# Performance work log

Measured on AMD Instinct MI355X. Metric: run time of the kernel, lower is better.

## Reference

```python
import math
import jax, jax.numpy as jnp
import numpy as np

EMB = 1024
HEADS = 16
HEAD_DIM = EMB // HEADS


def setup_inputs() -> dict:
    key = jax.random.key(0)
    ks = jax.random.split(key, 6)
    b, l = 4, 4096
    x = jax.random.normal(ks[0], (b, l, EMB), dtype=jnp.float32)
    # torch Linear weight shape (out, in); xavier_normal std = sqrt(2/(in+out))
    std = math.sqrt(2.0 / (EMB + EMB))
    Wq = jax.random.normal(ks[1], (EMB, EMB), dtype=jnp.float32) * std
    Wk = jax.random.normal(ks[2], (EMB, EMB), dtype=jnp.float32) * std
    Wv = jax.random.normal(ks[3], (EMB, EMB), dtype=jnp.float32) * std
    Wu = jax.random.normal(ks[4], (EMB, EMB), dtype=jnp.float32) * std
    Wo = jax.random.normal(ks[5], (EMB, EMB), dtype=jnp.float32) * std
    return {"x": x, "Wq": Wq, "Wk": Wk, "Wv": Wv, "Wu": Wu, "Wo": Wo}


def _srms_norm(x, eps=1e-12):
    # SRMSNorm over last dim with scale 1/sqrt(head_dims), computed in fp32
    dtype = x.dtype
    xf = x.astype(jnp.float32)
    scale = 1.0 / math.sqrt(x.shape[-1])
    n = jnp.linalg.norm(xf * scale, axis=-1, keepdims=True)
    return (xf / jnp.maximum(n, eps)).astype(dtype)


def reference(x, Wq, Wk, Wv, Wu, Wo):
    b, l, d = x.shape
    h, hd = HEADS, HEAD_DIM
    scale = math.sqrt(hd)

    def proj(W):
        return jnp.einsum('bld,ed->ble', x, W).reshape(b, l, h, hd).transpose(0, 2, 1, 3)

    q = jax.nn.relu(proj(Wq)) / scale        # (b,h,l,hd)
    k = jax.nn.relu(proj(Wk)) / scale
    v = proj(Wv)
    u = jax.nn.silu(proj(Wu))

    kv = jnp.einsum('bhlk,bhlv->bhkv', k, v)  # (b,h,hd,hd) state
    out = jnp.einsum('bhlk,bhkv->bhlv', q, kv)
    out = _srms_norm(out) * u
    out = out.transpose(0, 2, 1, 3).reshape(b, l, d)
    return jnp.einsum('bld,ed->ble', out, Wo)
```

## Files before the change

### kernel.cpp

```cpp
#include <hip/hip_runtime.h>

typedef _Float16 f16;
typedef _Float16 f16x4 __attribute__((ext_vector_type(4)));
typedef _Float16 f16x8 __attribute__((ext_vector_type(8)));
typedef float f32x4 __attribute__((ext_vector_type(4)));

#define EMB 1024
#define SEQL 4096
#define BATCH 4
#define NH 16
#define HD 64
#define BH 64
#define MROWS 16384
#define KVSPLIT 16

#define GLOAD_LDS(gp, lp) \
    __builtin_amdgcn_global_load_lds((const __attribute__((address_space(1))) void*)(gp), \
                                     (__attribute__((address_space(3))) void*)(lp), 16, 0, 0)

__global__ void cvt_kernel(const float* __restrict__ in, f16* __restrict__ out, int n4) {
    int i = blockIdx.x * blockDim.x + threadIdx.x;
    if (i < n4) {
        float4 v = ((const float4*)in)[i];
        f16x4 o = { (f16)v.x, (f16)v.y, (f16)v.z, (f16)v.w };
        ((f16x4*)out)[i] = o;
    }
}

struct WPtrs { const float* p[5]; };

__global__ void cvt_w_kernel(WPtrs wp, f16* __restrict__ out) {
    int i = blockIdx.x * blockDim.x + threadIdx.x;
    int wsel = blockIdx.y;
    const float4* src = (const float4*)wp.p[wsel];
    float4 v = src[i];
    f16x4 o = { (f16)v.x, (f16)v.y, (f16)v.z, (f16)v.w };
    ((f16x4*)(out + (size_t)wsel * EMB * EMB))[i] = o;
}

__global__ void zero_kernel(float4* __restrict__ p, int n4) {
    int i = blockIdx.x * blockDim.x + threadIdx.x;
    if (i < n4) p[i] = float4{0.f, 0.f, 0.f, 0.f};
}

template<int MODE>
__global__ __launch_bounds__(256) void gemm_kernel(
    const f16* __restrict__ A, const f16* __restrict__ Bt,
    void* __restrict__ Cv, int M, int N, int K)
{
    __shared__ f16 As[128 * 32];
    __shared__ f16 Bs[128 * 32];

    const int lane = threadIdx.x & 63;
    const int w    = threadIdx.x >> 6;
    const int rw   = lane & 15;
    const int quad = lane >> 4;
    const int m0 = blockIdx.y * 128;
    const int n0 = blockIdx.x * 128;
    const int mw = (w >> 1) * 64;
    const int nw = (w & 1) * 64;

    const int srow = lane >> 2;
    const int scol = (((lane & 3) ^ ((lane >> 3) & 3)) * 8);
    const f16* ag0 = A  + (size_t)(m0 + w * 16 + srow) * K + scol;
    const f16* ag1 = A  + (size_t)(m0 + 64 + w * 16 + srow) * K + scol;
    const f16* bg0 = Bt + (size_t)(n0 + w * 16 + srow) * K + scol;
    const f16* bg1 = Bt + (size_t)(n0 + 64 + w * 16 + srow) * K + scol;
    f16* la0 = &As[(w * 16) * 32];
    f16* la1 = &As[(64 + w * 16) * 32];
    f16* lb0 = &Bs[(w * 16) * 32];
    f16* lb1 = &Bs[(64 + w * 16) * 32];

    const int swz = (quad ^ ((rw >> 1) & 3)) * 8;

    f32x4 acc[4][4] = {};

    for (int k0 = 0; k0 < K; k0 += 32) {
        __syncthreads();
        GLOAD_LDS(ag0 + k0, la0);
        GLOAD_LDS(ag1 + k0, la1);
        GLOAD_LDS(bg0 + k0, lb0);
        GLOAD_LDS(bg1 + k0, lb1);
        __syncthreads();

        f16x8 af[4], bf[4];
        #pragma unroll
        for (int i = 0; i < 4; i++)
            af[i] = *(const f16x8*)&As[(mw + 16 * i + rw) * 32 + swz];
        #pragma unroll
        for (int j = 0; j < 4; j++)
            bf[j] = *(const f16x8*)&Bs[(nw + 16 * j + rw) * 32 + swz];
        #pragma unroll
        for (int i = 0; i < 4; i++)
            #pragma unroll
            for (int j = 0; j < 4; j++)
                acc[i][j] = __builtin_amdgcn_mfma_f32_16x16x32_f16(bf[j], af[i], acc[i][j], 0, 0, 0);
    }

    #pragma unroll
    for (int i = 0; i < 4; i++) {
        #pragma unroll
        for (int j = 0; j < 4; j++) {
            const int m_idx = m0 + mw + 16 * i + rw;
            const int n_idx = n0 + nw + 16 * j + quad * 4;
            if (MODE == 0) {
                float4 vv = { acc[i][j][0], acc[i][j][1], acc[i][j][2], acc[i][j][3] };
                *(float4*)&((float*)Cv)[(size_t)m_idx * N + n_idx] = vv;
            } else if (MODE == 3) {
                int sel = n_idx >> 10, e = n_idx & 1023;
                int b = m_idx >> 12, l = m_idx & 4095, h = e >> 6, hd = e & 63;
                f16x4 o;
                #pragma unroll
                for (int r = 0; r < 4; r++) {
                    float v = acc[i][j][r];
                    o[r] = (f16)(sel ? (v / (1.0f + __expf(-v))) : (fmaxf(v, 0.0f) * 0.125f));
                }
                *(f16x4*)&((f16*)Cv)[(size_t)sel * MROWS * EMB +
                                     (((size_t)(b * 16 + h) * 4096 + l) << 6) + hd] = o;
            } else {
                int sel = m_idx >> 10, e = m_idx & 1023;
                int b = n_idx >> 12, l = n_idx & 4095;
                f16x4 o;
                #pragma unroll
                for (int r = 0; r < 4; r++) {
                    float v = acc[i][j][r];
                    o[r] = (f16)(sel ? v : (fmaxf(v, 0.0f) * 0.125f));
                }
                *(f16x4*)&((f16*)Cv)[(size_t)sel * MROWS * EMB +
                                     (((size_t)b * 1024 + e) << 12) + l] = o;
            }
        }
    }
}

__global__ __launch_bounds__(256) void kv_split_kernel(
    const f16* __restrict__ kT, const f16* __restrict__ vT, float* __restrict__ kv32)
{
    const int bh    = blockIdx.x;
    const int chunk = blockIdx.y;
    const int lane  = threadIdx.x & 63;
    const int w     = threadIdx.x >> 6;
    const int rw    = lane & 15;
    const int quad  = lane >> 4;
    const int lbase = chunk * (SEQL / KVSPLIT);

    const f16* kp = kT + (size_t)bh * HD * SEQL + (size_t)(w * 16 + rw) * SEQL + lbase + quad * 8;
    const f16* vp = vT + (size_t)bh * HD * SEQL + (size_t)rw * SEQL + lbase + quad * 8;

    f32x4 acc[4] = {};
    for (int k0 = 0; k0 < SEQL / KVSPLIT; k0 += 32) {
        f16x8 a = *(const f16x8*)(kp + k0);
        #pragma unroll
        for (int t = 0; t < 4; t++) {
            f16x8 b = *(const f16x8*)(vp + (size_t)16 * t * SEQL + k0);
            acc[t] = __builtin_amdgcn_mfma_f32_16x16x32_f16(a, b, acc[t], 0, 0, 0);
        }
    }
    float* out = kv32 + (size_t)bh * HD * HD;
    #pragma unroll
    for (int t = 0; t < 4; t++)
        #pragma unroll
        for (int r = 0; r < 4; r++)
            atomicAdd(&out[(w * 16 + quad * 4 + r) * 64 + t * 16 + rw], acc[t][r]);
}

__global__ __launch_bounds__(256) void ret_out_kernel(
    const f16* __restrict__ q, const f16* __restrict__ u,
    const float* __restrict__ kv32, f16* __restrict__ o)
{
    const int bh    = blockIdx.x;
    const int chunk = blockIdx.y;
    const int lane  = threadIdx.x & 63;
    const int w     = threadIdx.x >> 6;
    const int rw    = lane & 15;
    const int quad  = lane >> 4;

    const float* kvp = kv32 + (size_t)bh * 4096;
    f16x8 bf[2][4];
    #pragma unroll
    for (int s = 0; s < 2; s++)
        #pragma unroll
        for (int t = 0; t < 4; t++)
            #pragma unroll
            for (int j = 0; j < 8; j++)
                bf[s][t][j] = (f16)kvp[(s * 32 + quad * 8 + j) * 64 + t * 16 + rw];

    const f16* qp = q + (size_t)bh * SEQL * HD;
    const f16* up = u + (size_t)bh * SEQL * HD;
    const int b = bh >> 4, h = bh & 15;
    f16* op = o + (size_t)b * SEQL * EMB + h * 64;

    const int l_wave = chunk * 512 + w * 128;
    for (int s = 0; s < 8; s++) {
        const int l0 = l_wave + s * 16;
        f16x8 a0 = *(const f16x8*)(qp + (size_t)(l0 + rw) * 64 + quad * 8);
        f16x8 a1 = *(const f16x8*)(qp + (size_t)(l0 + rw) * 64 + 32 + quad * 8);
        f32x4 acc[4] = {};
        #pragma unroll
        for (int t = 0; t < 4; t++) {
            acc[t] = __builtin_amdgcn_mfma_f32_16x16x32_f16(a0, bf[0][t], acc[t], 0, 0, 0);
            acc[t] = __builtin_amdgcn_mfma_f32_16x16x32_f16(a1, bf[1][t], acc[t], 0, 0, 0);
        }
        float inv[4];
        #pragma unroll
        for (int r = 0; r < 4; r++) {
            float ss = acc[0][r] * acc[0][r] + acc[1][r] * acc[1][r]
                     + acc[2][r] * acc[2][r] + acc[3][r] * acc[3][r];
            #pragma unroll
            for (int msk = 1; msk < 16; msk <<= 1)
                ss += __shfl_xor(ss, msk, 16);
            inv[r] = 8.0f / fmaxf(sqrtf(ss), 8e-12f);
        }
        #pragma unroll
        for (int t = 0; t < 4; t++)
            #pragma unroll
            for (int r = 0; r < 4; r++) {
                int l = l0 + quad * 4 + r;
                int col = t * 16 + rw;
                float uval = (float)up[(size_t)l * 64 + col];
                op[(size_t)l * EMB + col] = (f16)(acc[t][r] * inv[r] * uval);
            }
    }
}

extern "C" void kernel_launch(void* const* d_in, const int* in_sizes, int n_in,
                              void* d_out, int out_size, void* d_ws, size_t ws_size,
                              hipStream_t stream)
{
    const float* x = (const float*)d_in[0];
    WPtrs wp;
    wp.p[0] = (const float*)d_in[1];
    wp.p[1] = (const float*)d_in[4];
    wp.p[2] = (const float*)d_in[2];
    wp.p[3] = (const float*)d_in[3];
    wp.p[4] = (const float*)d_in[5];

    char* ws = (char*)d_ws;
    size_t off = 0;
    f16* x16 = (f16*)(ws + off); off += (size_t)MROWS * EMB * 2;
    f16* w16 = (f16*)(ws + off); off += (size_t)5 * EMB * EMB * 2;
    f16* qb  = (f16*)(ws + off); off += (size_t)MROWS * EMB * 2;
    f16* ub  = (f16*)(ws + off); off += (size_t)MROWS * EMB * 2;
    f16* kTb = (f16*)(ws + off); off += (size_t)MROWS * EMB * 2;
    f16* vTb = (f16*)(ws + off); off += (size_t)MROWS * EMB * 2;
    float* kv32 = (float*)(ws + off); off += (size_t)BH * HD * HD * 4;
    f16* ob  = x16;
    (void)ub; (void)vTb;

    cvt_kernel<<<(MROWS * EMB / 4) / 256, 256, 0, stream>>>(x, x16, MROWS * EMB / 4);
    cvt_w_kernel<<<dim3((EMB * EMB / 4) / 256, 5), 256, 0, stream>>>(wp, w16);
    zero_kernel<<<(BH * HD * HD / 4 + 255) / 256, 256, 0, stream>>>((float4*)kv32, BH * HD * HD / 4);

    f16* Wqu = w16;
    f16* Wkv = w16 + (size_t)2 * EMB * EMB;
    f16* Wo  = w16 + (size_t)4 * EMB * EMB;

    dim3 blk(256);
    gemm_kernel<3><<<dim3(16, 128), blk, 0, stream>>>(x16, Wqu, qb, MROWS, 2 * EMB, EMB);
    gemm_kernel<4><<<dim3(128, 16), blk, 0, stream>>>(Wkv, x16, kTb, 2 * EMB, MROWS, EMB);

    kv_split_kernel<<<dim3(BH, KVSPLIT), blk, 0, stream>>>(kTb, vTb, kv32);
    ret_out_kernel<<<dim3(BH, 8), blk, 0, stream>>>(qb, ub, kv32, ob);

    gemm_kernel<0><<<dim3(8, 128), blk, 0, stream>>>(ob, Wo, d_out, MROWS, EMB, EMB);
}
```

Baseline: 462.4 us.

## Rewrite GEMM as 256x256 tile, double-buffered, 8-wave pipelined kernel

```diff
diff --git a/kernel.cpp b/kernel.cpp
--- a/kernel.cpp
+++ b/kernel.cpp
@@ -43,94 +43,148 @@
     if (i < n4) p[i] = float4{0.f, 0.f, 0.f, 0.f};
 }
 
+
+#define FENCE asm volatile("" ::: "memory")
+#define WAITV(N) asm volatile("s_waitcnt vmcnt(" #N ")" ::: "memory")
+#define BAR do { FENCE; __builtin_amdgcn_s_barrier(); FENCE; } while (0)
+
 template<int MODE>
-__global__ __launch_bounds__(256) void gemm_kernel(
+__global__ __launch_bounds__(512, 2) void gemm_kernel(
     const f16* __restrict__ A, const f16* __restrict__ Bt,
     void* __restrict__ Cv, int M, int N, int K)
 {
-    __shared__ f16 As[128 * 32];
-    __shared__ f16 Bs[128 * 32];
-
-    const int lane = threadIdx.x & 63;
-    const int w    = threadIdx.x >> 6;
+    __shared__ f16 As[2][256 * 64];
+    __shared__ f16 Bs[2][256 * 64];
+
+    const int tid  = threadIdx.x;
+    const int lane = tid & 63;
+    const int w    = tid >> 6;
     const int rw   = lane & 15;
     const int quad = lane >> 4;
-    const int m0 = blockIdx.y * 128;
-    const int n0 = blockIdx.x * 128;
-    const int mw = (w >> 1) * 64;
-    const int nw = (w & 1) * 64;
-
-    const int srow = lane >> 2;
-    const int scol = (((lane & 3) ^ ((lane >> 3) & 3)) * 8);
-    const f16* ag0 = A  + (size_t)(m0 + w * 16 + srow) * K + scol;
-    const f16* ag1 = A  + (size_t)(m0 + 64 + w * 16 + srow) * K + scol;
-    const f16* bg0 = Bt + (size_t)(n0 + w * 16 + srow) * K + scol;
-    const f16* bg1 = Bt + (size_t)(n0 + 64 + w * 16 + srow) * K + scol;
-    f16* la0 = &As[(w * 16) * 32];
-    f16* la1 = &As[(64 + w * 16) * 32];
-    f16* lb0 = &Bs[(w * 16) * 32];
-    f16* lb1 = &Bs[(64 + w * 16) * 32];
-
-    const int swz = (quad ^ ((rw >> 1) & 3)) * 8;
-
-    f32x4 acc[4][4] = {};
-
-    for (int k0 = 0; k0 < K; k0 += 32) {
-        __syncthreads();
-        GLOAD_LDS(ag0 + k0, la0);
-        GLOAD_LDS(ag1 + k0, la1);
-        GLOAD_LDS(bg0 + k0, lb0);
-        GLOAD_LDS(bg1 + k0, lb1);
-        __syncthreads();
-
-        f16x8 af[4], bf[4];
-        #pragma unroll
-        for (int i = 0; i < 4; i++)
-            af[i] = *(const f16x8*)&As[(mw + 16 * i + rw) * 32 + swz];
-        #pragma unroll
-        for (int j = 0; j < 4; j++)
-            bf[j] = *(const f16x8*)&Bs[(nw + 16 * j + rw) * 32 + swz];
-        #pragma unroll
-        for (int i = 0; i < 4; i++)
-            #pragma unroll
-            for (int j = 0; j < 4; j++)
-                acc[i][j] = __builtin_amdgcn_mfma_f32_16x16x32_f16(bf[j], af[i], acc[i][j], 0, 0, 0);
-    }
-
-    #pragma unroll
-    for (int i = 0; i < 4; i++) {
-        #pragma unroll
-        for (int j = 0; j < 4; j++) {
-            const int m_idx = m0 + mw + 16 * i + rw;
-            const int n_idx = n0 + nw + 16 * j + quad * 4;
-            if (MODE == 0) {
-                float4 vv = { acc[i][j][0], acc[i][j][1], acc[i][j][2], acc[i][j][3] };
-                *(float4*)&((float*)Cv)[(size_t)m_idx * N + n_idx] = vv;
-            } else if (MODE == 3) {
-                int sel = n_idx >> 10, e = n_idx & 1023;
-                int b = m_idx >> 12, l = m_idx & 4095, h = e >> 6, hd = e & 63;
-                f16x4 o;
-                #pragma unroll
-                for (int r = 0; r < 4; r++) {
-                    float v = acc[i][j][r];
-                    o[r] = (f16)(sel ? (v / (1.0f + __expf(-v))) : (fmaxf(v, 0.0f) * 0.125f));
-                }
-                *(f16x4*)&((f16*)Cv)[(size_t)sel * MROWS * EMB +
-                                     (((size_t)(b * 16 + h) * 4096 + l) << 6) + hd] = o;
-            } else {
-                int sel = m_idx >> 10, e = m_idx & 1023;
-                int b = n_idx >> 12, l = n_idx & 4095;
-                f16x4 o;
-                #pragma unroll
-                for (int r = 0; r < 4; r++) {
-                    float v = acc[i][j][r];
-                    o[r] = (f16)(sel ? v : (fmaxf(v, 0.0f) * 0.125f));
-                }
-                *(f16x4*)&((f16*)Cv)[(size_t)sel * MROWS * EMB +
-                                     (((size_t)b * 1024 + e) << 12) + l] = o;
+    const int wm   = w >> 2;
+    const int wn   = w & 3;
+    const int m0 = blockIdx.y * 256;
+    const int n0 = blockIdx.x * 256;
+    const size_t Ks = (size_t)K;
+    const int NT = K >> 6;
+
+    const int srow8 = lane >> 3;
+    const int slog  = (lane & 7) ^ srow8;
+    const f16* gA = A  + (size_t)(m0 + w * 8 + srow8) * Ks + slog * 8;
+    const f16* gB = Bt + (size_t)(n0 + w * 8 + srow8) * Ks + slog * 8;
+    const int lst = w * 512;
+
+#define STAGE_A(H, T, BUF) do { \
+    GLOAD_LDS(gA + (size_t)((H) * 128 +  0) * Ks + (T) * 64, &As[BUF][(H) * 8192 + lst]); \
+    GLOAD_LDS(gA + (size_t)((H) * 128 + 64) * Ks + (T) * 64, &As[BUF][(H) * 8192 + 4096 + lst]); \
+} while (0)
+#define STAGE_B(H, T, BUF) do { \
+    GLOAD_LDS(gB + (size_t)((H) * 128 +  0) * Ks + (T) * 64, &Bs[BUF][(H) * 8192 + lst]); \
+    GLOAD_LDS(gB + (size_t)((H) * 128 + 64) * Ks + (T) * 64, &Bs[BUF][(H) * 8192 + 4096 + lst]); \
+} while (0)
+
+    const int rw7   = rw & 7;
+    const int s0o   = ( quad      ^ rw7) * 8;
+    const int s1o   = ((quad + 4) ^ rw7) * 8;
+    const int abase = (wm * 64 + rw) * 64;
+    const int bbase = (wn * 32 + rw) * 64;
+
+    f32x4 acc[2][2][4][2] = {};
+    f16x8 af[4][2], bf[2][2];
+
+#define READ_A(QM, BUF) do { \
+    _Pragma("unroll") \
+    for (int mi = 0; mi < 4; ++mi) { \
+        af[mi][0] = *(const f16x8*)&As[BUF][(QM) * 8192 + abase + mi * 1024 + s0o]; \
+        af[mi][1] = *(const f16x8*)&As[BUF][(QM) * 8192 + abase + mi * 1024 + s1o]; \
+    } \
+} while (0)
+#define READ_B(QN, BUF) do { \
+    _Pragma("unroll") \
+    for (int nj = 0; nj < 2; ++nj) { \
+        bf[nj][0] = *(const f16x8*)&Bs[BUF][(QN) * 8192 + bbase + nj * 1024 + s0o]; \
+        bf[nj][1] = *(const f16x8*)&Bs[BUF][(QN) * 8192 + bbase + nj * 1024 + s1o]; \
+    } \
+} while (0)
+#define MFMA_Q(QM, QN) do { \
+    __builtin_amdgcn_s_setprio(1); \
+    _Pragma("unroll") \
+    for (int mi = 0; mi < 4; ++mi) \
+        _Pragma("unroll") \
+        for (int nj = 0; nj < 2; ++nj) { \
+            acc[QM][QN][mi][nj] = __builtin_amdgcn_mfma_f32_16x16x32_f16(bf[nj][0], af[mi][0], acc[QM][QN][mi][nj], 0, 0, 0); \
+            acc[QM][QN][mi][nj] = __builtin_amdgcn_mfma_f32_16x16x32_f16(bf[nj][1], af[mi][1], acc[QM][QN][mi][nj], 0, 0, 0); \
+        } \
+    __builtin_amdgcn_s_setprio(0); \
+} while (0)
+
+    STAGE_A(0, 0, 0);
+    STAGE_B(0, 0, 0);
+    STAGE_B(1, 0, 0);
+    STAGE_A(1, 0, 0);
+    if (NT > 1) { STAGE_A(0, 1, 1); WAITV(2); } else { WAITV(0); }
+    BAR;
+
+    for (int kt = 0; kt < NT; ++kt) {
+        const int cur = kt & 1, nxt = cur ^ 1;
+        const bool p1 = (kt + 1 < NT), p2 = (kt + 2 < NT);
+        READ_A(0, cur); READ_B(0, cur);
+        if (p1) { STAGE_B(0, kt + 1, nxt); WAITV(6); } else { WAITV(2); }
+        BAR; MFMA_Q(0, 0); BAR;
+        READ_B(1, cur);
+        if (p1) { STAGE_B(1, kt + 1, nxt); WAITV(6); } else { WAITV(0); }
+        BAR; MFMA_Q(0, 1); BAR;
+        READ_A(1, cur);
+        if (p1) { STAGE_A(1, kt + 1, nxt); WAITV(6); } else { WAITV(0); }
+        BAR; MFMA_Q(1, 1); BAR;
+        READ_B(0, cur);
+        if (p2) { STAGE_A(0, kt + 2, cur); WAITV(6); } else { WAITV(4); }
+        BAR; MFMA_Q(1, 0); BAR;
+    }
+
+    #pragma unroll
+    for (int qm = 0; qm < 2; ++qm)
+    #pragma unroll
+    for (int qn = 0; qn < 2; ++qn)
+    #pragma unroll
+    for (int mi = 0; mi < 4; ++mi)
+    #pragma unroll
+    for (int nj = 0; nj < 2; ++nj) {
+        const int m_idx = m0 + qm * 128 + wm * 64 + mi * 16 + rw;
+        const int n_idx = n0 + qn * 128 + wn * 32 + nj * 16 + quad * 4;
+        f32x4 a = acc[qm][qn][mi][nj];
+        if (MODE == 0) {
+            float4 vv = { a[0], a[1], a[2], a[3] };
+            *(float4*)&((float*)Cv)[(size_t)m_idx * N + n_idx] = vv;
+        } else if (MODE == 3) {
+            int sel = n_idx >> 10, e = n_idx & 1023;
+            int b = m_idx >> 12, l = m_idx & 4095, h = e >> 6, hdi = e & 63;
+            f16x4 o;
+            #pragma unroll
+            for (int r = 0; r < 4; r++) {
+                float v = a[r];
+                o[r] = (f16)(sel ? (v / (1.0f + __expf(-v))) : (fmaxf(v, 0.0f) * 0.125f));
             }
+            *(f16x4*)&((f16*)Cv)[(size_t)sel * MROWS * EMB +
+                                 (((size_t)(b * 16 + h) * 4096 + l) << 6) + hdi] = o;
+        } else {
+            int sel = m_idx >> 10, e = m_idx & 1023;
+            int b = n_idx >> 12, l = n_idx & 4095;
+            f16x4 o;
+            #pragma unroll
+            for (int r = 0; r < 4; r++) {
+                float v = a[r];
+                o[r] = (f16)(sel ? v : (fmaxf(v, 0.0f) * 0.125f));
+            }
+            *(f16x4*)&((f16*)Cv)[(size_t)sel * MROWS * EMB +
+                                 (((size_t)b * 1024 + e) << 12) + l] = o;
         }
     }
+#undef STAGE_A
+#undef STAGE_B
+#undef READ_A
+#undef READ_B
+#undef MFMA_Q
 }
 
 __global__ __launch_bounds__(256) void kv_split_kernel(
@@ -255,12 +309,12 @@
     f16* Wkv = w16 + (size_t)2 * EMB * EMB;
     f16* Wo  = w16 + (size_t)4 * EMB * EMB;
 
-    dim3 blk(256);
-    gemm_kernel<3><<<dim3(16, 128), blk, 0, stream>>>(x16, Wqu, qb, MROWS, 2 * EMB, EMB);
-    gemm_kernel<4><<<dim3(128, 16), blk, 0, stream>>>(Wkv, x16, kTb, 2 * EMB, MROWS, EMB);
-
-    kv_split_kernel<<<dim3(BH, KVSPLIT), blk, 0, stream>>>(kTb, vTb, kv32);
-    ret_out_kernel<<<dim3(BH, 8), blk, 0, stream>>>(qb, ub, kv32, ob);
-
-    gemm_kernel<0><<<dim3(8, 128), blk, 0, stream>>>(ob, Wo, d_out, MROWS, EMB, EMB);
-}
+    dim3 blk(512);
+    gemm_kernel<3><<<dim3(8, 64), blk, 0, stream>>>(x16, Wqu, qb, MROWS, 2 * EMB, EMB);
+    gemm_kernel<4><<<dim3(64, 8), blk, 0, stream>>>(Wkv, x16, kTb, 2 * EMB, MROWS, EMB);
+
+    kv_split_kernel<<<dim3(BH, KVSPLIT), dim3(256), 0, stream>>>(kTb, vTb, kv32);
+    ret_out_kernel<<<dim3(BH, 8), dim3(256), 0, stream>>>(qb, ub, kv32, ob);
+
+    gemm_kernel<0><<<dim3(4, 64), blk, 0, stream>>>(ob, Wo, d_out, MROWS, EMB, EMB);
+}
```

Measured after the change: 395.0 us. -14.6%, faster.
